# Kernel tuning notes

Hardware: AMD Instinct MI355X
Metric: run time of the kernel (lower is better)

## Reference

```python
import jax, jax.numpy as jnp
import numpy as np

B = 4        # number of point clouds (equal-size contiguous batches)
P = 8192     # points per cloud
C_IN = 64
C_OUT = 64
K = 16       # kNN neighbors (includes the point itself, as in PyG knn)
EPS = 1e-5
NEG_SLOPE = 0.2


def setup_inputs() -> dict:
    key = jax.random.key(0)
    k1, k2, k3 = jax.random.split(key, 3)
    x = jax.random.normal(k1, (B * P, C_IN), dtype=jnp.float32)
    batch = jnp.repeat(jnp.arange(B, dtype=jnp.int64), P)  # sorted, equal sizes
    W = jax.random.normal(k2, (2 * C_IN, C_OUT), dtype=jnp.float32) * (1.0 / np.sqrt(2 * C_IN))
    b = jax.random.normal(k3, (C_OUT,), dtype=jnp.float32) * 0.01
    gamma = jnp.ones((C_OUT,), dtype=jnp.float32)
    beta = jnp.zeros((C_OUT,), dtype=jnp.float32)
    return {"x": x, "batch": batch, "W": W, "b": b, "gamma": gamma, "beta": beta}


def _edgeconv(x, W, b, gamma, beta):
    xb = x.reshape(B, P, C_IN)
    # per-cloud pairwise squared distances: [B, P, P]
    sq = jnp.sum(xb * xb, axis=-1)
    d = sq[:, :, None] + sq[:, None, :] - 2.0 * jnp.einsum("bpc,bqc->bpq", xb, xb)
    # k nearest neighbors (smallest distance, self included)
    _, idx = jax.lax.top_k(-d, K)                      # [B, P, K]
    xj = jax.vmap(lambda pts, ind: pts[ind])(xb, idx)  # [B, P, K, C_IN]
    xi = xb[:, :, None, :]
    e = jnp.concatenate([jnp.broadcast_to(xi, xj.shape), xj - xi], axis=-1)  # [B,P,K,2C]
    # edge MLP: Linear -> BatchNorm1d (training-mode batch stats over all edges) -> LeakyReLU
    h = jnp.einsum("bpke,eo->bpko", e, W) + b          # [B, P, K, C_OUT]
    hf = h.reshape(-1, C_OUT)
    mean = jnp.mean(hf, axis=0)
    var = jnp.mean(hf * hf, axis=0) - mean * mean      # biased variance (torch BN)
    hn = (h - mean) * jax.lax.rsqrt(var + EPS) * gamma + beta
    a = jnp.where(hn >= 0, hn, NEG_SLOPE * hn)
    # max aggregation over neighbors
    return jnp.max(a, axis=2).reshape(B * P, C_OUT)


def reference(x, batch, W, b, gamma, beta):
    # `batch` encodes B equal-size contiguous clouds; kNN is computed per cloud.
    return _edgeconv(x, W, b, gamma, beta)
```

## Files before the change

kernel.cpp:

```cpp
#include <hip/hip_runtime.h>
#include <cfloat>

#define BATCH 4
#define P 8192
#define C 64
#define KNN 16
#define NPTS (BATCH * P)
#define NEDGE (NPTS * KNN)
#define EPSV 1e-5f
#define SLOPE 0.2f
#define NQ 2
#define QCOLS (P / NQ)
#define NCH (QCOLS / 64)
#define CAP 52

typedef __attribute__((ext_vector_type(8))) short bf16x8;
typedef __attribute__((ext_vector_type(16))) float f32x16;


__device__ __forceinline__ unsigned short f2bf(float f) {
    unsigned u = __float_as_uint(f);
    u += 0x7FFFu + ((u >> 16) & 1u);
    return (unsigned short)(u >> 16);
}
__device__ __forceinline__ float bf2f(unsigned short s) {
    return __uint_as_float(((unsigned)s) << 16);
}
__device__ __forceinline__ unsigned monof(float f) {
    unsigned u = __float_as_uint(f);
    return u ^ ((unsigned)((int)u >> 31) | 0x80000000u);
}
__device__ __forceinline__ float invmonof(unsigned k) {
    unsigned u = (k & 0x80000000u) ? (k ^ 0x80000000u) : ~k;
    return __uint_as_float(u);
}

__global__ void prep_frag(const float* __restrict__ x, uint4* __restrict__ xfh,
                          uint4* __restrict__ xfm, uint4* __restrict__ xfl,
                          float* __restrict__ sq) {
    __shared__ float part[32][9];
    int tid = threadIdx.x;
    int ptl = tid >> 3, j8 = tid & 7;
    int g = blockIdx.x;
    int p = g * 32 + ptl;
    const float4* xp = (const float4*)(x + (size_t)p * C + j8 * 8);
    float4 a = xp[0], b = xp[1];
    float v[8] = {a.x, a.y, a.z, a.w, b.x, b.y, b.z, b.w};
    unsigned short hs[8], ms[8], ls[8];
    float ssum = 0.f;
#pragma unroll
    for (int e = 0; e < 8; ++e) {
        float xv = v[e];
        ssum = fmaf(xv, xv, ssum);
        unsigned short h = f2bf(xv);
        float r1 = xv - bf2f(h);
        unsigned short m = f2bf(r1);
        float r2 = r1 - bf2f(m);
        unsigned short l = f2bf(r2);
        hs[e] = h; ms[e] = m; ls[e] = l;
    }
    int dst = (g * 4 + (j8 >> 1)) * 64 + ptl + 32 * (j8 & 1);
    uint4 ph, pm, pl;
    ph.x = (unsigned)hs[0] | ((unsigned)hs[1] << 16);
    ph.y = (unsigned)hs[2] | ((unsigned)hs[3] << 16);
    ph.z = (unsigned)hs[4] | ((unsigned)hs[5] << 16);
    ph.w = (unsigned)hs[6] | ((unsigned)hs[7] << 16);
    pm.x = (unsigned)ms[0] | ((unsigned)ms[1] << 16);
    pm.y = (unsigned)ms[2] | ((unsigned)ms[3] << 16);
    pm.z = (unsigned)ms[4] | ((unsigned)ms[5] << 16);
    pm.w = (unsigned)ms[6] | ((unsigned)ms[7] << 16);
    pl.x = (unsigned)ls[0] | ((unsigned)ls[1] << 16);
    pl.y = (unsigned)ls[2] | ((unsigned)ls[3] << 16);
    pl.z = (unsigned)ls[4] | ((unsigned)ls[5] << 16);
    pl.w = (unsigned)ls[6] | ((unsigned)ls[7] << 16);
    xfh[dst] = ph; xfm[dst] = pm; xfl[dst] = pl;
    part[ptl][j8] = ssum;
    __syncthreads();
    if (j8 == 0) {
        float s = 0.f;
#pragma unroll
        for (int k = 0; k < 8; ++k) s += part[ptl][k];
        sq[p] = s;
    }
}

__global__ __launch_bounds__(256, 4) void knn_kernel(const uint4* __restrict__ xfh,
                                                     const uint4* __restrict__ xfm,
                                                     const uint4* __restrict__ xfl,
                                                     const float* __restrict__ sq,
                                                     float* __restrict__ pv,
                                                     int* __restrict__ pi) {
    __shared__ unsigned long long bufk[64 * CAP];
    __shared__ unsigned long long topk[64 * 16];
    __shared__ float worstL[64];
    __shared__ int   cnt[64];

    int tid = threadIdx.x;
    int b = blockIdx.x & 3;
    int t = blockIdx.x >> 2;
    int tile = t & 127;
    int half = t >> 7;
    int bglob = b * P;
    int r0 = tile * 64;
    int colbase = half * QCOLS;
    int w = tid >> 6, lane = tid & 63;
    int wr = w & 1, wc = w >> 1;

    if (tid < 64) cnt[tid] = 0;

    int gA = ((bglob + r0) >> 5) + wr;
    bf16x8 Ah[4], Am[4], Al[4];
#pragma unroll
    for (int kk = 0; kk < 4; ++kk) {
        Ah[kk] = __builtin_bit_cast(bf16x8, xfh[(gA * 4 + kk) * 64 + lane]);
        Am[kk] = __builtin_bit_cast(bf16x8, xfm[(gA * 4 + kk) * 64 + lane]);
        Al[kk] = __builtin_bit_cast(bf16x8, xfl[(gA * 4 + kk) * 64 + lane]);
    }

    int rbase = wr * 32 + 4 * (lane >> 5);
    int colq = wc * 32 + (lane & 31);

    for (int chunk = 0; chunk < NCH; ++chunk) {
        int c0 = colbase + chunk * 64;
        int gB = ((bglob + c0) >> 5) + wc;
        bf16x8 Bh[4], Bm[4], Bl[4];
#pragma unroll
        for (int kk = 0; kk < 4; ++kk) {
            Bh[kk] = __builtin_bit_cast(bf16x8, xfh[(gB * 4 + kk) * 64 + lane]);
            Bm[kk] = __builtin_bit_cast(bf16x8, xfm[(gB * 4 + kk) * 64 + lane]);
            Bl[kk] = __builtin_bit_cast(bf16x8, xfl[(gB * 4 + kk) * 64 + lane]);
        }
        float sc = sq[bglob + c0 + colq];

        f32x16 acc0, acc1;
#pragma unroll
        for (int i = 0; i < 16; ++i) { acc0[i] = 0.f; acc1[i] = 0.f; }
#pragma unroll
        for (int kk = 0; kk < 4; ++kk) {
            acc0 = __builtin_amdgcn_mfma_f32_32x32x16_bf16(Ah[kk], Bh[kk], acc0, 0, 0, 0);
            acc1 = __builtin_amdgcn_mfma_f32_32x32x16_bf16(Ah[kk], Bm[kk], acc1, 0, 0, 0);
            acc0 = __builtin_amdgcn_mfma_f32_32x32x16_bf16(Am[kk], Bh[kk], acc0, 0, 0, 0);
            acc1 = __builtin_amdgcn_mfma_f32_32x32x16_bf16(Am[kk], Bm[kk], acc1, 0, 0, 0);
            acc0 = __builtin_amdgcn_mfma_f32_32x32x16_bf16(Ah[kk], Bl[kk], acc0, 0, 0, 0);
            acc1 = __builtin_amdgcn_mfma_f32_32x32x16_bf16(Al[kk], Bh[kk], acc1, 0, 0, 0);
        }

        int colg = bglob + c0 + colq;
        if (chunk == 0) {
#pragma unroll
            for (int reg = 0; reg < 16; ++reg) {
                float s = fmaf(-2.f, acc0[reg] + acc1[reg], sc);
                int row = rbase + (reg & 3) + 8 * (reg >> 2);
                unsigned long long key =
                    ((unsigned long long)monof(s) << 32) | (unsigned)colg;
                if (colq < 16) topk[row * 16 + colq] = key;
                else           bufk[row * CAP + (colq - 16)] = key;
            }
        } else {
            float4 twA[4];
#pragma unroll
            for (int g4 = 0; g4 < 4; ++g4)
                twA[g4] = *(const float4*)&worstL[rbase + 8 * g4];
#pragma unroll
            for (int reg = 0; reg < 16; ++reg) {
                float s = fmaf(-2.f, acc0[reg] + acc1[reg], sc);
                float tW = ((const float*)&twA[reg >> 2])[reg & 3];
                if (s < tW) {
                    int row = rbase + (reg & 3) + 8 * (reg >> 2);
                    int slot = atomicAdd(&cnt[row], 1);
                    if (slot < CAP)
                        bufk[row * CAP + slot] =
                            ((unsigned long long)monof(s) << 32) | (unsigned)colg;
                }
            }
        }

        if ((chunk & (chunk + 1)) == 0) {
            __syncthreads();
            for (int rr = 0; rr < 16; ++rr) {
                int row = w * 16 + rr;
                int n = (chunk == 0) ? 48 : (cnt[row] < CAP ? cnt[row] : CAP);
                unsigned long long mykey;
                if (lane < 16)            mykey = topk[row * 16 + lane];
                else if (lane < 16 + n)   mykey = bufk[row * CAP + (lane - 16)];
                else                      mykey = ~0ull;
                int rank = 0;
#pragma unroll
                for (int j = 0; j < 16; ++j)
                    rank += (topk[row * 16 + j] < mykey) ? 1 : 0;
                for (int j = 0; j < n; ++j)
                    rank += (bufk[row * CAP + j] < mykey) ? 1 : 0;
                if (rank < 16) topk[row * 16 + rank] = mykey;
                if (rank == 15) worstL[row] = invmonof((unsigned)(mykey >> 32));
                if (lane == 0) cnt[row] = 0;
            }
            __syncthreads();
        }
    }

    for (int rr = 0; rr < 16; ++rr) {
        int row = w * 16 + rr;
        if (lane < 16) {
            unsigned long long k = topk[row * 16 + lane];
            size_t o = (((size_t)(bglob + r0 + row)) * NQ + half) * KNN;
            pv[o + lane] = invmonof((unsigned)(k >> 32));
            pi[o + lane] = (int)(unsigned)(k & 0xFFFFFFFFu);
        }
    }
}

__global__ void merge_kernel(const float* __restrict__ pv, const int* __restrict__ pi,
                             int* __restrict__ idx_out) {
    __shared__ float mv[128 * 33];
    __shared__ int   mi[128 * 33];
    int tid = threadIdx.x;
    int lr = tid & 127, q = tid >> 7;
    int row = blockIdx.x * 128 + lr;
    size_t o = ((size_t)row * NQ + q) * KNN;
#pragma unroll
    for (int j = 0; j < 16; ++j) {
        mv[lr * 33 + q * 16 + j] = pv[o + j];
        mi[lr * 33 + q * 16 + j] = pi[o + j];
    }
    __syncthreads();
    if (tid < 128) {
        float tv[16];
        int ti[16];
        float worst = FLT_MAX;
#pragma unroll
        for (int j = 0; j < 16; ++j) { tv[j] = FLT_MAX; ti[j] = 0; }
        for (int e = 0; e < 32; ++e) {
            float s = mv[tid * 33 + e];
            if (s < worst) {
                float mx = tv[0];
                int pos = 0;
#pragma unroll
                for (int j = 1; j < 16; ++j) {
                    bool g = tv[j] > mx;
                    mx = g ? tv[j] : mx;
                    pos = g ? j : pos;
                }
#pragma unroll
                for (int j = 0; j < 16; ++j)
                    if (j == pos) { tv[j] = s; ti[j] = mi[tid * 33 + e]; }
                float nw = tv[0];
#pragma unroll
                for (int j = 1; j < 16; ++j) nw = fmaxf(nw, tv[j]);
                worst = nw;
            }
        }
        size_t oo = (size_t)row * KNN;
#pragma unroll
        for (int j = 0; j < 16; ++j) idx_out[oo + j] = ti[j];
    }
}

__global__ void prep_UV(const float* __restrict__ x, const float* __restrict__ W,
                        float* __restrict__ U, float* __restrict__ V) {
    __shared__ float Ws[128][64];
    __shared__ float xs[4][64];
    int tid = threadIdx.x;
    for (int i = tid; i < 128 * 64; i += 256) ((float*)Ws)[i] = W[i];
    int p0 = blockIdx.x * 4;
    int r = tid >> 6, c = tid & 63;
    xs[r][c] = x[(size_t)(p0 + r) * C + c];
    __syncthreads();
    float u = 0.f, v = 0.f;
#pragma unroll
    for (int k = 0; k < 64; ++k) {
        float xv = xs[r][k];
        float w1 = Ws[k][c];
        float w2 = Ws[64 + k][c];
        u = fmaf(xv, w1 - w2, u);
        v = fmaf(xv, w2, v);
    }
    size_t o = (size_t)(p0 + r) * C + c;
    U[o] = u;
    V[o] = v;
}

__global__ void stats_kernel(const float* __restrict__ U, const float* __restrict__ V,
                             const float* __restrict__ bias, const int* __restrict__ idx,
                             float* __restrict__ stats) {
    int tid = threadIdx.x;
    int c = tid & 63, kk = tid >> 6;
    int p0 = blockIdx.x * 32;
    float bc = bias[c];
    float sum = 0.f, sumsq = 0.f;
    for (int pp = 0; pp < 32; ++pp) {
        int p = p0 + pp;
        float u = U[(size_t)p * C + c] + bc;
#pragma unroll
        for (int k4 = 0; k4 < 4; ++k4) {
            int j = idx[(size_t)p * KNN + kk * 4 + k4];
            float h = u + V[(size_t)j * C + c];
            sum += h;
            sumsq = fmaf(h, h, sumsq);
        }
    }
    __shared__ float red[2][4][64];
    red[0][kk][c] = sum;
    red[1][kk][c] = sumsq;
    __syncthreads();
    if (tid < 64) {
        float s = red[0][0][tid] + red[0][1][tid] + red[0][2][tid] + red[0][3][tid];
        atomicAdd(&stats[tid], s);
    } else if (tid < 128) {
        int cc = tid - 64;
        float s = red[1][0][cc] + red[1][1][cc] + red[1][2][cc] + red[1][3][cc];
        atomicAdd(&stats[64 + cc], s);
    }
}

__global__ void finalize_kernel(const float* __restrict__ stats,
                                const float* __restrict__ gamma,
                                const float* __restrict__ beta,
                                float* __restrict__ sshift) {
    int c = threadIdx.x;
    const float N = (float)NEDGE;
    float mean = stats[c] / N;
    float var = stats[64 + c] / N - mean * mean;
    float s = gamma[c] * rsqrtf(var + EPSV);
    sshift[c] = s;
    sshift[64 + c] = beta[c] - mean * s;
}

__global__ void out_kernel(const float* __restrict__ U, const float* __restrict__ V,
                           const float* __restrict__ bias, const int* __restrict__ idx,
                           const float* __restrict__ sshift, float* __restrict__ out) {
    int tid = threadIdx.x;
    int c = tid & 63, g = tid >> 6;
    int p0 = blockIdx.x * 16;
    float s = sshift[c], t = sshift[64 + c];
    float bc = bias[c];
    for (int pp = g; pp < 16; pp += 4) {
        int p = p0 + pp;
        float mx = -FLT_MAX, mn = FLT_MAX;
#pragma unroll
        for (int k = 0; k < KNN; ++k) {
            int j = idx[(size_t)p * KNN + k];
            float v = V[(size_t)j * C + c];
            mx = fmaxf(mx, v);
            mn = fminf(mn, v);
        }
        float hsel = (s >= 0.f) ? mx : mn;
        float hn = fmaf(s, U[(size_t)p * C + c] + bc + hsel, t);
        out[(size_t)p * C + c] = (hn >= 0.f) ? hn : SLOPE * hn;
    }
}

extern "C" void kernel_launch(void* const* d_in, const int* in_sizes, int n_in,
                              void* d_out, int out_size, void* d_ws, size_t ws_size,
                              hipStream_t stream) {
    const float* x     = (const float*)d_in[0];
    const float* W     = (const float*)d_in[2];
    const float* bias  = (const float*)d_in[3];
    const float* gamma = (const float*)d_in[4];
    const float* beta  = (const float*)d_in[5];
    float* out = (float*)d_out;

    float* wsf    = (float*)d_ws;
    float* U      = wsf;
    float* V      = wsf + 2097152;
    uint4* xfh    = (uint4*)wsf;
    uint4* xfm    = (uint4*)(wsf + 1048576);
    uint4* xfl    = (uint4*)(wsf + 2097152);
    float* sq     = wsf + 4194304;
    float* stats  = wsf + 4227072;
    float* sshift = wsf + 4227200;
    int*   idx    = (int*)(wsf + 4227328);
    float* pv     = wsf + 4751616;
    int*   pi     = (int*)(wsf + 5800192);

    hipLaunchKernelGGL(prep_frag, dim3(NPTS / 32), dim3(256), 0, stream, x, xfh, xfm, xfl, sq);
    hipLaunchKernelGGL(knn_kernel, dim3(BATCH * (P / 64) * NQ), dim3(256), 0, stream,
                       (const uint4*)xfh, (const uint4*)xfm, (const uint4*)xfl, sq, pv, pi);
    hipLaunchKernelGGL(merge_kernel, dim3(NPTS / 128), dim3(256), 0, stream, pv, pi, idx);
    hipLaunchKernelGGL(prep_UV, dim3(NPTS / 4), dim3(256), 0, stream, x, W, U, V);
    hipMemsetAsync(stats, 0, 128 * sizeof(float), stream);
    hipLaunchKernelGGL(stats_kernel, dim3(NPTS / 32), dim3(256), 0, stream, U, V, bias, idx, stats);
    hipLaunchKernelGGL(finalize_kernel, dim3(1), dim3(64), 0, stream, stats, gamma, beta, sshift);
    hipLaunchKernelGGL(out_kernel, dim3(NPTS / 16), dim3(256), 0, stream, U, V, bias, idx, sshift, out);
}
```

Measured before the change: 599.2 us.

## Replace shared-memory candidate buffering with per-lane register top-k in kNN kernel

The kNN kernel swaps operands so that each lane owns one query row and scans 32-column chunks across a 2048-column slice per wave. Each lane keeps a 16-entry register top-k of packed (distance, index) keys with a threshold test, replacing the shared-memory candidate buffer, atomics and the periodic block-wide rank merges. Per-lane lists are merged through shared memory at the end, and the merge kernel now compares packed 64-bit keys so ties break deterministically. The cost is heavy register pressure (launch bounds lowered to 2 blocks) and divergent scalar insertion work, while the column operands are streamed straight from global memory with no reuse across waves.

```diff
diff --git a/kernel.cpp b/kernel.cpp
--- a/kernel.cpp
+++ b/kernel.cpp
@@ -11,11 +11,11 @@
 #define SLOPE 0.2f
 #define NQ 2
 #define QCOLS (P / NQ)
-#define NCH (QCOLS / 64)
-#define CAP 52
 
 typedef __attribute__((ext_vector_type(8))) short bf16x8;
 typedef __attribute__((ext_vector_type(16))) float f32x16;
+
+#define KSENT 0xFF7FFFFFFFFFFFFFull
 
 
 __device__ __forceinline__ unsigned short f2bf(float f) {
@@ -84,16 +84,46 @@
     }
 }
 
-__global__ __launch_bounds__(256, 4) void knn_kernel(const uint4* __restrict__ xfh,
+#define TRYINSK(KV)                                                           \
+    if ((KV) < worstk) {                                                      \
+        unsigned long long mx = tk[0]; int pos = 0;                           \
+        _Pragma("unroll")                                                     \
+        for (int j = 1; j < 16; ++j) {                                        \
+            bool g = tk[j] > mx; mx = g ? tk[j] : mx; pos = g ? j : pos;      \
+        }                                                                     \
+        _Pragma("unroll")                                                     \
+        for (int j = 0; j < 16; ++j)                                          \
+            if (j == pos) tk[j] = (KV);                                       \
+        unsigned long long nw = tk[0];                                        \
+        _Pragma("unroll")                                                     \
+        for (int j = 1; j < 16; ++j) nw = (tk[j] > nw) ? tk[j] : nw;          \
+        worstk = nw;                                                          \
+    }
+
+#define TRYINSKW(KV)                                                          \
+    if ((KV) < worstk) {                                                      \
+        unsigned long long mx = tk[0]; int pos = 0;                           \
+        _Pragma("unroll")                                                     \
+        for (int j = 1; j < 16; ++j) {                                        \
+            bool g = tk[j] > mx; mx = g ? tk[j] : mx; pos = g ? j : pos;      \
+        }                                                                     \
+        _Pragma("unroll")                                                     \
+        for (int j = 0; j < 16; ++j)                                          \
+            if (j == pos) tk[j] = (KV);                                       \
+        unsigned long long nw = tk[0];                                        \
+        _Pragma("unroll")                                                     \
+        for (int j = 1; j < 16; ++j) nw = (tk[j] > nw) ? tk[j] : nw;          \
+        worstk = nw;                                                          \
+        worstf = invmonof((unsigned)(worstk >> 32));                          \
+    }
+
+__global__ __launch_bounds__(256, 2) void knn_kernel(const uint4* __restrict__ xfh,
                                                      const uint4* __restrict__ xfm,
                                                      const uint4* __restrict__ xfl,
                                                      const float* __restrict__ sq,
                                                      float* __restrict__ pv,
                                                      int* __restrict__ pi) {
-    __shared__ unsigned long long bufk[64 * CAP];
-    __shared__ unsigned long long topk[64 * 16];
-    __shared__ float worstL[64];
-    __shared__ int   cnt[64];
+    __shared__ unsigned long long fink[64][65];
 
     int tid = threadIdx.x;
     int b = blockIdx.x & 3;
@@ -102,156 +132,144 @@
     int half = t >> 7;
     int bglob = b * P;
     int r0 = tile * 64;
-    int colbase = half * QCOLS;
     int w = tid >> 6, lane = tid & 63;
     int wr = w & 1, wc = w >> 1;
-
-    if (tid < 64) cnt[tid] = 0;
+    int hi = lane >> 5;
+    int rloc = lane & 31;
 
     int gA = ((bglob + r0) >> 5) + wr;
-    bf16x8 Ah[4], Am[4], Al[4];
+    bf16x8 Rh[4], Rm[4], Rl[4];
 #pragma unroll
     for (int kk = 0; kk < 4; ++kk) {
-        Ah[kk] = __builtin_bit_cast(bf16x8, xfh[(gA * 4 + kk) * 64 + lane]);
-        Am[kk] = __builtin_bit_cast(bf16x8, xfm[(gA * 4 + kk) * 64 + lane]);
-        Al[kk] = __builtin_bit_cast(bf16x8, xfl[(gA * 4 + kk) * 64 + lane]);
-    }
-
-    int rbase = wr * 32 + 4 * (lane >> 5);
-    int colq = wc * 32 + (lane & 31);
-
-    for (int chunk = 0; chunk < NCH; ++chunk) {
-        int c0 = colbase + chunk * 64;
-        int gB = ((bglob + c0) >> 5) + wc;
-        bf16x8 Bh[4], Bm[4], Bl[4];
+        Rh[kk] = __builtin_bit_cast(bf16x8, xfh[(gA * 4 + kk) * 64 + lane]);
+        Rm[kk] = __builtin_bit_cast(bf16x8, xfm[(gA * 4 + kk) * 64 + lane]);
+        Rl[kk] = __builtin_bit_cast(bf16x8, xfl[(gA * 4 + kk) * 64 + lane]);
+    }
+
+    unsigned long long tk[16];
+#pragma unroll
+    for (int j = 0; j < 16; ++j) tk[j] = KSENT;
+    unsigned long long worstk = KSENT;
+    float worstf = FLT_MAX;
+
+    int cw0 = half * QCOLS + wc * 2048;
+
+    for (int chunk = 0; chunk < 64; ++chunk) {
+        int c0 = cw0 + chunk * 32;
+        int gB = (bglob + c0) >> 5;
+        const uint4* ch = &xfh[(gB * 4) * 64 + lane];
+        const uint4* cm = &xfm[(gB * 4) * 64 + lane];
+        const uint4* cl = &xfl[(gB * 4) * 64 + lane];
+
+        f32x16 acc0, acc1;
+#pragma unroll
+        for (int i = 0; i < 16; ++i) { acc0[i] = 0.f; acc1[i] = 0.f; }
 #pragma unroll
         for (int kk = 0; kk < 4; ++kk) {
-            Bh[kk] = __builtin_bit_cast(bf16x8, xfh[(gB * 4 + kk) * 64 + lane]);
-            Bm[kk] = __builtin_bit_cast(bf16x8, xfm[(gB * 4 + kk) * 64 + lane]);
-            Bl[kk] = __builtin_bit_cast(bf16x8, xfl[(gB * 4 + kk) * 64 + lane]);
-        }
-        float sc = sq[bglob + c0 + colq];
-
-        f32x16 acc0, acc1;
-#pragma unroll
-        for (int i = 0; i < 16; ++i) { acc0[i] = 0.f; acc1[i] = 0.f; }
-#pragma unroll
-        for (int kk = 0; kk < 4; ++kk) {
-            acc0 = __builtin_amdgcn_mfma_f32_32x32x16_bf16(Ah[kk], Bh[kk], acc0, 0, 0, 0);
-            acc1 = __builtin_amdgcn_mfma_f32_32x32x16_bf16(Ah[kk], Bm[kk], acc1, 0, 0, 0);
-            acc0 = __builtin_amdgcn_mfma_f32_32x32x16_bf16(Am[kk], Bh[kk], acc0, 0, 0, 0);
-            acc1 = __builtin_amdgcn_mfma_f32_32x32x16_bf16(Am[kk], Bm[kk], acc1, 0, 0, 0);
-            acc0 = __builtin_amdgcn_mfma_f32_32x32x16_bf16(Ah[kk], Bl[kk], acc0, 0, 0, 0);
-            acc1 = __builtin_amdgcn_mfma_f32_32x32x16_bf16(Al[kk], Bh[kk], acc1, 0, 0, 0);
-        }
-
-        int colg = bglob + c0 + colq;
-        if (chunk == 0) {
-#pragma unroll
-            for (int reg = 0; reg < 16; ++reg) {
-                float s = fmaf(-2.f, acc0[reg] + acc1[reg], sc);
-                int row = rbase + (reg & 3) + 8 * (reg >> 2);
+            bf16x8 Ch = __builtin_bit_cast(bf16x8, ch[kk * 64]);
+            bf16x8 Cm = __builtin_bit_cast(bf16x8, cm[kk * 64]);
+            bf16x8 Cl = __builtin_bit_cast(bf16x8, cl[kk * 64]);
+            acc0 = __builtin_amdgcn_mfma_f32_32x32x16_bf16(Ch, Rh[kk], acc0, 0, 0, 0);
+            acc1 = __builtin_amdgcn_mfma_f32_32x32x16_bf16(Ch, Rm[kk], acc1, 0, 0, 0);
+            acc0 = __builtin_amdgcn_mfma_f32_32x32x16_bf16(Cm, Rh[kk], acc0, 0, 0, 0);
+            acc1 = __builtin_amdgcn_mfma_f32_32x32x16_bf16(Cm, Rm[kk], acc1, 0, 0, 0);
+            acc0 = __builtin_amdgcn_mfma_f32_32x32x16_bf16(Ch, Rl[kk], acc0, 0, 0, 0);
+            acc1 = __builtin_amdgcn_mfma_f32_32x32x16_bf16(Cl, Rh[kk], acc1, 0, 0, 0);
+        }
+
+        int cb = c0 + 4 * hi;
+        float4 sqA[4];
+#pragma unroll
+        for (int g4 = 0; g4 < 4; ++g4)
+            sqA[g4] = *(const float4*)(&sq[bglob + cb + g4 * 8]);
+        int bgc = bglob + cb;
+
+#pragma unroll
+        for (int reg = 0; reg < 16; ++reg) {
+            float s = fmaf(-2.f, acc0[reg] + acc1[reg],
+                           ((const float*)&sqA[reg >> 2])[reg & 3]);
+            if (s <= worstf) {
+                int cgl = bgc + (reg & 3) + 8 * (reg >> 2);
                 unsigned long long key =
-                    ((unsigned long long)monof(s) << 32) | (unsigned)colg;
-                if (colq < 16) topk[row * 16 + colq] = key;
-                else           bufk[row * CAP + (colq - 16)] = key;
+                    ((unsigned long long)monof(s) << 32) | (unsigned)cgl;
+                TRYINSKW(key)
             }
-        } else {
-            float4 twA[4];
-#pragma unroll
-            for (int g4 = 0; g4 < 4; ++g4)
-                twA[g4] = *(const float4*)&worstL[rbase + 8 * g4];
-#pragma unroll
-            for (int reg = 0; reg < 16; ++reg) {
-                float s = fmaf(-2.f, acc0[reg] + acc1[reg], sc);
-                float tW = ((const float*)&twA[reg >> 2])[reg & 3];
-                if (s < tW) {
-                    int row = rbase + (reg & 3) + 8 * (reg >> 2);
-                    int slot = atomicAdd(&cnt[row], 1);
-                    if (slot < CAP)
-                        bufk[row * CAP + slot] =
-                            ((unsigned long long)monof(s) << 32) | (unsigned)colg;
-                }
-            }
-        }
-
-        if ((chunk & (chunk + 1)) == 0) {
-            __syncthreads();
-            for (int rr = 0; rr < 16; ++rr) {
-                int row = w * 16 + rr;
-                int n = (chunk == 0) ? 48 : (cnt[row] < CAP ? cnt[row] : CAP);
-                unsigned long long mykey;
-                if (lane < 16)            mykey = topk[row * 16 + lane];
-                else if (lane < 16 + n)   mykey = bufk[row * CAP + (lane - 16)];
-                else                      mykey = ~0ull;
-                int rank = 0;
-#pragma unroll
-                for (int j = 0; j < 16; ++j)
-                    rank += (topk[row * 16 + j] < mykey) ? 1 : 0;
-                for (int j = 0; j < n; ++j)
-                    rank += (bufk[row * CAP + j] < mykey) ? 1 : 0;
-                if (rank < 16) topk[row * 16 + rank] = mykey;
-                if (rank == 15) worstL[row] = invmonof((unsigned)(mykey >> 32));
-                if (lane == 0) cnt[row] = 0;
-            }
-            __syncthreads();
-        }
-    }
-
-    for (int rr = 0; rr < 16; ++rr) {
-        int row = w * 16 + rr;
-        if (lane < 16) {
-            unsigned long long k = topk[row * 16 + lane];
-            size_t o = (((size_t)(bglob + r0 + row)) * NQ + half) * KNN;
-            pv[o + lane] = invmonof((unsigned)(k >> 32));
-            pi[o + lane] = (int)(unsigned)(k & 0xFFFFFFFFu);
+        }
+    }
+
+    {
+        int rowl = 32 * wr + rloc;
+        int li = wc * 2 + hi;
+#pragma unroll
+        for (int j = 0; j < 16; ++j) fink[rowl][li * 16 + j] = tk[j];
+    }
+    __syncthreads();
+    if (tid < 128) {
+        int row = tid & 63, pr = tid >> 6;
+        int base = pr * 32;
+        unsigned long long tk[16];
+#pragma unroll
+        for (int j = 0; j < 16; ++j) tk[j] = fink[row][base + j];
+        unsigned long long worstk = tk[0];
+#pragma unroll
+        for (int j = 1; j < 16; ++j) worstk = (tk[j] > worstk) ? tk[j] : worstk;
+        for (int e = 0; e < 16; ++e) {
+            unsigned long long k = fink[row][base + 16 + e];
+            TRYINSK(k)
+        }
+#pragma unroll
+        for (int j = 0; j < 16; ++j) fink[row][base + j] = tk[j];
+    }
+    __syncthreads();
+    if (tid < 64) {
+        int row = tid;
+        unsigned long long tk[16];
+#pragma unroll
+        for (int j = 0; j < 16; ++j) tk[j] = fink[row][j];
+        unsigned long long worstk = tk[0];
+#pragma unroll
+        for (int j = 1; j < 16; ++j) worstk = (tk[j] > worstk) ? tk[j] : worstk;
+        for (int e = 0; e < 16; ++e) {
+            unsigned long long k = fink[row][32 + e];
+            TRYINSK(k)
+        }
+        size_t o = (((size_t)(bglob + r0 + row)) * NQ + half) * KNN;
+#pragma unroll
+        for (int j = 0; j < 16; ++j) {
+            pv[o + j] = invmonof((unsigned)(tk[j] >> 32));
+            pi[o + j] = (int)(unsigned)(tk[j] & 0xFFFFFFFFu);
         }
     }
 }
 
 __global__ void merge_kernel(const float* __restrict__ pv, const int* __restrict__ pi,
                              int* __restrict__ idx_out) {
-    __shared__ float mv[128 * 33];
-    __shared__ int   mi[128 * 33];
+    __shared__ unsigned long long mk[128 * 33];
     int tid = threadIdx.x;
     int lr = tid & 127, q = tid >> 7;
     int row = blockIdx.x * 128 + lr;
     size_t o = ((size_t)row * NQ + q) * KNN;
 #pragma unroll
     for (int j = 0; j < 16; ++j) {
-        mv[lr * 33 + q * 16 + j] = pv[o + j];
-        mi[lr * 33 + q * 16 + j] = pi[o + j];
+        mk[lr * 33 + q * 16 + j] =
+            ((unsigned long long)monof(pv[o + j]) << 32) | (unsigned)pi[o + j];
     }
     __syncthreads();
     if (tid < 128) {
-        float tv[16];
-        int ti[16];
-        float worst = FLT_MAX;
-#pragma unroll
-        for (int j = 0; j < 16; ++j) { tv[j] = FLT_MAX; ti[j] = 0; }
-        for (int e = 0; e < 32; ++e) {
-            float s = mv[tid * 33 + e];
-            if (s < worst) {
-                float mx = tv[0];
-                int pos = 0;
-#pragma unroll
-                for (int j = 1; j < 16; ++j) {
-                    bool g = tv[j] > mx;
-                    mx = g ? tv[j] : mx;
-                    pos = g ? j : pos;
-                }
-#pragma unroll
-                for (int j = 0; j < 16; ++j)
-                    if (j == pos) { tv[j] = s; ti[j] = mi[tid * 33 + e]; }
-                float nw = tv[0];
-#pragma unroll
-                for (int j = 1; j < 16; ++j) nw = fmaxf(nw, tv[j]);
-                worst = nw;
-            }
-        }
-        size_t oo = (size_t)row * KNN;
-#pragma unroll
-        for (int j = 0; j < 16; ++j) idx_out[oo + j] = ti[j];
+        unsigned long long tk[16];
+#pragma unroll
+        for (int j = 0; j < 16; ++j) tk[j] = mk[tid * 33 + j];
+        unsigned long long worstk = tk[0];
+#pragma unroll
+        for (int j = 1; j < 16; ++j) worstk = (tk[j] > worstk) ? tk[j] : worstk;
+        for (int e = 16; e < 32; ++e) {
+            unsigned long long k = mk[tid * 33 + e];
+            TRYINSK(k)
+        }
+        size_t oo = (size_t)tid * KNN + (size_t)blockIdx.x * 128 * KNN;
+#pragma unroll
+        for (int j = 0; j < 16; ++j)
+            idx_out[oo + j] = (int)(unsigned)(tk[j] & 0xFFFFFFFFu);
     }
 }
 
```

Measured after the change: 1.321 ms. +120.5%, slower.
